# Kernel tuning notes

Hardware: AMD Instinct MI355X
Metric: run time of the kernel (lower is better)

## Reference

```python
import jax, jax.numpy as jnp
import numpy as np
from jax import lax

K = 3  # deform kernel size (forced by shape consistency of the offset branch)


def conv2d(x, w, b, pad):
    y = lax.conv_general_dilated(x, w, (1, 1), [(pad, pad), (pad, pad)],
                                 dimension_numbers=('NCHW', 'OIHW', 'NCHW'))
    return y + b[None, :, None, None]


def deform_conv(x, offset, w):
    # Deformable conv v1, stride 1, pad 0, per-group offsets, zero outside borders.
    B, Cin, H, W = x.shape
    Cout = w.shape[0]
    Ho, Wo = H - K + 1, W - K + 1
    G = offset.shape[1] // (2 * K * K)  # num deformable groups (= cin // c_p_g)
    cpg = Cin // G
    # offset layout: [B, G, K*K, 2(y,x), Ho, Wo]
    off = offset.reshape(B, G, K * K, 2, Ho, Wo)
    ky = (jnp.arange(K * K) // K).astype(x.dtype)
    kx = (jnp.arange(K * K) % K).astype(x.dtype)
    py = off[:, :, :, 0] + jnp.arange(Ho, dtype=x.dtype)[None, None, None, :, None] + ky[None, None, :, None, None]
    px = off[:, :, :, 1] + jnp.arange(Wo, dtype=x.dtype)[None, None, None, None, :] + kx[None, None, :, None, None]
    y0 = jnp.floor(py)
    x0 = jnp.floor(px)
    fy = (py - y0)[..., None]  # [B,G,KK,Ho,Wo,1]
    fx = (px - x0)[..., None]
    y0i = y0.astype(jnp.int32)
    x0i = x0.astype(jnp.int32)
    xr = x.reshape(B, G, cpg, H, W)
    bi = jnp.arange(B)[:, None, None, None, None]
    gi = jnp.arange(G)[None, :, None, None, None]

    def gather(iy, ix):
        valid = (iy >= 0) & (iy < H) & (ix >= 0) & (ix < W)
        v = xr[bi, gi, :, jnp.clip(iy, 0, H - 1), jnp.clip(ix, 0, W - 1)]  # [B,G,KK,Ho,Wo,cpg]
        return v * valid[..., None].astype(x.dtype)

    v = ((1 - fy) * (1 - fx) * gather(y0i, x0i)
         + (1 - fy) * fx * gather(y0i, x0i + 1)
         + fy * (1 - fx) * gather(y0i + 1, x0i)
         + fy * fx * gather(y0i + 1, x0i + 1))
    # [B,G,KK,Ho,Wo,cpg] -> [B, Cin*K*K, Ho, Wo] matching weight layout [Cout, Cin, K, K]
    cols = v.transpose(0, 1, 5, 2, 3, 4).reshape(B, Cin * K * K, Ho, Wo)
    return jnp.einsum('ok,bkhw->bohw', w.reshape(Cout, -1), cols)


def setup_inputs() -> dict:
    key = jax.random.key(0)
    ks = jax.random.split(key, 8)
    B, cin, cout, H, W = 4, 64, 64, 130, 130
    s = 0.05
    x = jax.random.normal(ks[0], (B, cin, H, W), jnp.float32)
    w0 = jax.random.normal(ks[1], (cin, cin, 3, 3), jnp.float32) * s
    b0 = jnp.zeros((cin,), jnp.float32)
    w1 = jax.random.normal(ks[2], (cin // 2, cin, 1, 1), jnp.float32) * s
    b1 = jnp.zeros((cin // 2,), jnp.float32)
    w2 = jax.random.normal(ks[3], (cin // 2, cin // 2, 3, 3), jnp.float32) * s
    b2 = jnp.zeros((cin // 2,), jnp.float32)
    off_ch = cin * 2 * K * K  # c_p_g = 1 -> G = cin
    w3 = jax.random.normal(ks[4], (off_ch, cin // 2, 1, 1), jnp.float32) * s
    b3 = jnp.zeros((off_ch,), jnp.float32)
    wd = jax.random.normal(ks[5], (cout, cin, K, K), jnp.float32) * s
    return {"x": x, "w0": w0, "b0": b0, "w1": w1, "b1": b1, "w2": w2, "b2": b2,
            "w3": w3, "b3": b3, "wd": wd}


def reference(x, w0, b0, w1, b1, w2, b2, w3, b3, wd):
    t = conv2d(x, w0, b0, 0)                                   # [B,cin,H-2,W-2]
    t = lax.reduce_window(t, -jnp.inf, lax.max, (1, 1, 2, 2), (1, 1, 2, 2), 'VALID')
    t = conv2d(t, w1, b1, 0)
    t = conv2d(t, w2, b2, 1)
    t = conv2d(t, w3, b3, 0)                                   # offset logits
    t = jnp.repeat(jnp.repeat(t, 2, axis=2), 2, axis=3)        # nearest x2 upsample
    return deform_conv(x, t, wd)
```

## Files before the change

kernel.cpp:

```cpp
#include <hip/hip_runtime.h>
#include <hip/hip_bf16.h>
#include <hip/hip_fp16.h>


#define HX 130
#define WX 130

typedef short bf16x8 __attribute__((ext_vector_type(8)));
typedef _Float16 f16x8 __attribute__((ext_vector_type(8)));
typedef float f32x4 __attribute__((ext_vector_type(4)));

static __device__ __forceinline__ unsigned short f2bf(float f) {
    unsigned u = __float_as_uint(f);
    unsigned r = u + 0x7fff + ((u >> 16) & 1);
    return (unsigned short)(r >> 16);
}

static __device__ __forceinline__ int aoff320(int row, int col) {
    return row * 320 + ((((col >> 3) ^ (row & 7))) << 3) + (col & 7);
}

static __device__ __forceinline__ int aoff192(int row, int col) {
    return row * 192 + ((((col >> 3) ^ (row & 7))) << 3) + (col & 7);
}

static __device__ __forceinline__ int aoff80(int row, int col) {
    return row * 80 + ((((col >> 3) ^ (row & 7))) << 3) + (col & 7);
}

__global__ __launch_bounds__(256) void k_wdt(const float* __restrict__ wd,
                                             const float* __restrict__ w3,
                                             const float* __restrict__ w0,
                                             const float* __restrict__ w2,
                                             const float* __restrict__ w1,
                                             unsigned short* __restrict__ wdtb,
                                             __half* __restrict__ w3h,
                                             unsigned short* __restrict__ w0b,
                                             unsigned short* __restrict__ w2b,
                                             unsigned short* __restrict__ w1b) {
    int idx = blockIdx.x * 256 + threadIdx.x;
    if (idx < 36864) {
        int o = idx / 576;
        int rem = idx - o * 576;
        int c = rem / 9;
        int kk = rem - c * 9;
        int h = c >> 5;
        int c5 = c & 31;
        int col = (c5 >> 4) * 144 + ((c5 >> 3) & 1) * 72 + (c5 & 7) * 9 + kk;
        wdtb[(size_t)(h * 64 + o) * 288 + col] = f2bf(wd[idx]);
        if (idx < 16) wdtb[36864 + idx] = 0;
    } else if (idx < 73728) {
        int i2 = idx - 36864;
        w3h[i2] = __float2half_rn(w3[i2]);
    } else if (idx < 114688) {
        int i3 = idx - 73728;
        int row = i3 / 160;
        int col = i3 - row * 160;
        int cig = row >> 6, oc = row & 63;
        unsigned short v = 0;
        if (col < 144) {
            int ci = (col * 57) >> 9;
            int kk = col - ci * 9;
            v = f2bf(w0[(size_t)(oc * 64 + cig * 16 + ci) * 9 + kk]);
        }
        w0b[i3] = v;
    } else if (idx < 124928) {
        int i4 = idx - 114688;
        int row = i4 / 160;
        int col = i4 - row * 160;
        int cig = row >> 5, oc = row & 31;
        unsigned short v = 0;
        if (col < 144) {
            int ci = (col * 57) >> 9;
            int kk = col - ci * 9;
            v = f2bf(w2[(size_t)(oc * 32 + cig * 16 + ci) * 9 + kk]);
        }
        w2b[i4] = v;
    } else {
        int i5 = idx - 124928;
        w1b[i5] = f2bf(w1[i5]);
    }
}

__global__ __launch_bounds__(256, 4) void k_conv0_mfma(const float* __restrict__ x,
                                                       const unsigned short* __restrict__ w0b,
                                                       const float* __restrict__ b0,
                                                       float* __restrict__ p1) {
    int blk = blockIdx.x;
    int tx = blk & 15;
    int ty = (blk >> 4) & 15;
    int b = blk >> 8;
    int tid = threadIdx.x;
    int w = tid >> 6;
    int lane = tid & 63;
    int lm = lane & 15;
    int lq = lane >> 4;
    int oy0 = ty * 8, ox0 = tx * 8;

    __shared__ __align__(16) unsigned short alds[64 * 192];
    __shared__ __align__(16) float xlds[1600];

    f32x4 acc[4];
    #pragma unroll
    for (int n = 0; n < 4; ++n) acc[n] = (f32x4){0.f, 0.f, 0.f, 0.f};

    if (tid < 128) {
        *(bf16x8*)&alds[aoff192(tid >> 1, 144 + (tid & 1) * 8)] =
            (bf16x8){0, 0, 0, 0, 0, 0, 0, 0};
    }

    const float* xb = x + (size_t)(b * 64) * (HX * WX) + oy0 * WX + ox0;
    int apx = tid >> 2;
    int acq = tid & 3;
    int py = apx >> 3, pxx = apx & 7;

    for (int cig = 0; cig < 4; ++cig) {
        #pragma unroll
        for (int j = 0; j < 7; ++j) {
            int i = tid + j * 256;
            if (i < 1600) {
                int ci = i / 100;
                int rem = i - ci * 100;
                int rr = rem / 10, cc = rem - rr * 10;
                xlds[i] = xb[(size_t)(cig * 16 + ci) * (HX * WX) + rr * WX + cc];
            }
        }
        __syncthreads();
        #pragma unroll
        for (int jj = 0; jj < 36; ++jj) {
            int col = acq * 36 + jj;
            int ci = (col * 57) >> 9;
            int kk = col - ci * 9;
            int ky = kk / 3, kx = kk - ky * 3;
            alds[aoff192(apx, col)] =
                f2bf(xlds[ci * 100 + (py + ky) * 10 + (pxx + kx)]);
        }
        __syncthreads();
        int arow = w * 16 + lm;
        const unsigned short* bbase = w0b + (size_t)cig * 64 * 160;
        #pragma unroll
        for (int ks = 0; ks < 5; ++ks) {
            bf16x8 a = *(const bf16x8*)&alds[aoff192(arow, ks * 32 + lq * 8)];
            #pragma unroll
            for (int n = 0; n < 4; ++n) {
                bf16x8 bb = *(const bf16x8*)(bbase + (size_t)(n * 16 + lm) * 160
                                             + ks * 32 + lq * 8);
                acc[n] = __builtin_amdgcn_mfma_f32_16x16x32_bf16(a, bb, acc[n], 0, 0, 0);
            }
        }
    }

    __syncthreads();
    float* dlds = (float*)alds;
    #pragma unroll
    for (int n = 0; n < 4; ++n) {
        int oc = n * 16 + lm;
        #pragma unroll
        for (int r = 0; r < 4; ++r) {
            int px = w * 16 + lq * 4 + r;
            dlds[oc * 65 + px] = acc[n][r];
        }
    }
    __syncthreads();
    {
        int oc = tid >> 2;
        int ppy = tid & 3;
        float bo = b0[oc];
        float4 o4;
        #pragma unroll
        for (int ppx = 0; ppx < 4; ++ppx) {
            const float* dp = &dlds[oc * 65 + (2 * ppy) * 8 + 2 * ppx];
            float m = fmaxf(fmaxf(dp[0], dp[1]), fmaxf(dp[8], dp[9])) + bo;
            ((float*)&o4)[ppx] = m;
        }
        *(float4*)(p1 + (((size_t)b * 64 + oc) * 64 + ty * 4 + ppy) * 64 + tx * 4) = o4;
    }
}

__global__ __launch_bounds__(256) void k_conv13(const float* __restrict__ p1,
                                                const unsigned short* __restrict__ w1b,
                                                const float* __restrict__ b1,
                                                const unsigned short* __restrict__ w2b,
                                                const float* __restrict__ b2,
                                                float* __restrict__ t3) {
    int blk = blockIdx.x;
    int tx = blk & 7;
    int ty = (blk >> 3) & 7;
    int b = blk >> 6;
    int tid = threadIdx.x;
    int w = tid >> 6;
    int lane = tid & 63;
    int lm = lane & 15;
    int lq = lane >> 4;
    int oy0 = ty * 8, ox0 = tx * 8;

    __shared__ __align__(16) float t2b[32 * 100];
    __shared__ __align__(16) unsigned short areg[64 * 192];

    const float* pb = p1 + (size_t)(b * 64) * 4096;
    #pragma unroll
    for (int j = 0; j < 25; ++j) {
        int i = tid + j * 256;
        int ci = i / 100;
        int pp = i - ci * 100;
        int rr = pp / 10, cc = pp - rr * 10;
        int gy = oy0 + rr - 1, gx = ox0 + cc - 1;
        bool ok = (gy >= 0) & (gy < 64) & (gx >= 0) & (gx < 64);
        float v = ok ? pb[(size_t)ci * 4096 + gy * 64 + gx] : 0.f;
        areg[aoff80(pp, ci)] = f2bf(v);
    }
    __syncthreads();

    #pragma unroll
    for (int s7 = 0; s7 < 2; ++s7) {
        int rt = w + s7 * 4;
        if (rt < 7) {
            f32x4 a1[2];
            a1[0] = (f32x4){0.f, 0.f, 0.f, 0.f};
            a1[1] = (f32x4){0.f, 0.f, 0.f, 0.f};
            #pragma unroll
            for (int ks = 0; ks < 2; ++ks) {
                bf16x8 a = *(const bf16x8*)&areg[aoff80(rt * 16 + lm, ks * 32 + lq * 8)];
                #pragma unroll
                for (int n = 0; n < 2; ++n) {
                    bf16x8 bb = *(const bf16x8*)(w1b + (size_t)(n * 16 + lm) * 64
                                                 + ks * 32 + lq * 8);
                    a1[n] = __builtin_amdgcn_mfma_f32_16x16x32_bf16(a, bb, a1[n], 0, 0, 0);
                }
            }
            #pragma unroll
            for (int n = 0; n < 2; ++n) {
                int oc = n * 16 + lm;
                float bv = b1[oc];
                #pragma unroll
                for (int r = 0; r < 4; ++r) {
                    int px = rt * 16 + lq * 4 + r;
                    if (px < 100) t2b[oc * 100 + px] = a1[n][r] + bv;
                }
            }
        }
    }
    __syncthreads();

    int apx = tid >> 2, acq = tid & 3;
    int py = apx >> 3, pxx = apx & 7;
    f32x4 acc3[2];
    acc3[0] = (f32x4){0.f, 0.f, 0.f, 0.f};
    acc3[1] = (f32x4){0.f, 0.f, 0.f, 0.f};
    if (tid < 128) {
        *(bf16x8*)&areg[aoff192(tid >> 1, 144 + (tid & 1) * 8)] =
            (bf16x8){0, 0, 0, 0, 0, 0, 0, 0};
    }
    #pragma unroll 1
    for (int cig = 0; cig < 2; ++cig) {
        __syncthreads();
        #pragma unroll
        for (int jj = 0; jj < 36; ++jj) {
            int col = acq * 36 + jj;
            int ci = (col * 57) >> 9;
            int kk = col - ci * 9;
            int ky = kk / 3, kx = kk - ky * 3;
            areg[aoff192(apx, col)] =
                f2bf(t2b[(cig * 16 + ci) * 100 + (py + ky) * 10 + (pxx + kx)]);
        }
        __syncthreads();
        int arow = w * 16 + lm;
        const unsigned short* bbase = w2b + (size_t)cig * 32 * 160;
        #pragma unroll
        for (int ks = 0; ks < 5; ++ks) {
            bf16x8 a = *(const bf16x8*)&areg[aoff192(arow, ks * 32 + lq * 8)];
            #pragma unroll
            for (int n = 0; n < 2; ++n) {
                bf16x8 bb = *(const bf16x8*)(bbase + (size_t)(n * 16 + lm) * 160
                                             + ks * 32 + lq * 8);
                acc3[n] = __builtin_amdgcn_mfma_f32_16x16x32_bf16(a, bb, acc3[n], 0, 0, 0);
            }
        }
    }

    __syncthreads();
    float* dlds = (float*)areg;
    #pragma unroll
    for (int n = 0; n < 2; ++n) {
        int oc = n * 16 + lm;
        #pragma unroll
        for (int r = 0; r < 4; ++r) {
            int px = w * 16 + lq * 4 + r;
            dlds[oc * 65 + px] = acc3[n][r];
        }
    }
    __syncthreads();
    {
        int oc = tid >> 3;
        int r = tid & 7;
        float bo = b2[oc];
        const float* dp = &dlds[oc * 65 + r * 8];
        float* op = t3 + ((size_t)(b * 32 + oc) * 64 + oy0 + r) * 64 + ox0;
        float4 a4 = make_float4(dp[0] + bo, dp[1] + bo, dp[2] + bo, dp[3] + bo);
        float4 b4 = make_float4(dp[4] + bo, dp[5] + bo, dp[6] + bo, dp[7] + bo);
        *(float4*)(op) = a4;
        *(float4*)(op + 4) = b4;
    }
}

__global__ __launch_bounds__(256, 3) void k_deform(const float* __restrict__ x,
                                                   const float* __restrict__ t3,
                                                   const __half* __restrict__ w3h,
                                                   const float* __restrict__ b3,
                                                   const unsigned short* __restrict__ wdtb,
                                                   float* __restrict__ out) {
    int blk = blockIdx.x;
    int k8 = blk & 7;
    int j8 = blk >> 3;
    int b = k8 & 3;
    int strip = j8 * 2 + (k8 >> 2);
    int tid = threadIdx.x;
    int po0 = strip * 16;
    int qy = po0 >> 6;
    int qx0 = po0 & 63;
    int w = tid >> 6;
    int lane = tid & 63;
    int lm = lane & 15;
    int lq = lane >> 4;
    int tq = tid & 15;
    int kb = tid >> 4;

    __shared__ __align__(16) unsigned short alds[64 * 320];
    __shared__ __align__(16) __half2 soff[2304];
    __shared__ __align__(16) _Float16 st3t[16 * 40];

    f32x4 acc[4];
    #pragma unroll
    for (int n = 0; n < 4; ++n) acc[n] = (f32x4){0.f, 0.f, 0.f, 0.f};

    const float* xb = x + (size_t)b * 64 * HX * WX;
    float fybase = (float)(2 * qy);
    float fxbase = (float)(2 * (qx0 + tq));

    {
        int px = tid & 15, ci0 = tid >> 4;
        const float* t3p = t3 + (size_t)b * 32 * 4096 + (qy * 64 + qx0 + px);
        st3t[px * 40 + ci0]      = (_Float16)t3p[(size_t)ci0 * 4096];
        st3t[px * 40 + ci0 + 16] = (_Float16)t3p[(size_t)(ci0 + 16) * 4096];
    }
    __syncthreads();
    const f16x8 bfrag = *(const f16x8*)&st3t[lm * 40 + lq * 8];

    for (int h = 0; h < 2; ++h) {
        #pragma unroll 1
        for (int sl = 0; sl < 2; ++sl) {
            int s = h * 2 + sl;
            __syncthreads();

            #pragma unroll
            for (int rep = 0; rep < 5; ++rep) {
                int t = rep * 4 + w;
                if (rep == 4) { if (w >= 2) break; t = 16 + w; }
                const f16x8 afrag = *(const f16x8*)((const _Float16*)w3h
                        + (size_t)(s * 288 + t * 16 + lm) * 32 + lq * 8);
                f32x4 d = __builtin_amdgcn_mfma_f32_16x16x32_f16(
                        afrag, bfrag, (f32x4){0.f, 0.f, 0.f, 0.f}, 0, 0, 0);
                float4 bq = *(const float4*)(b3 + s * 288 + t * 16 + lq * 4);
                int p0 = (t * 8 + lq * 2) * 16 + lm;
                soff[p0]      = __floats2half2_rn(d[0] + bq.x, d[1] + bq.y);
                soff[p0 + 16] = __floats2half2_rn(d[2] + bq.z, d[3] + bq.w);
            }
            __syncthreads();

            __half2 o2h[9];
            #pragma unroll
            for (int it = 0; it < 9; ++it)
                o2h[it] = soff[it * 256 + tid];
            #pragma unroll
            for (int it = 0; it < 9; ++it) {
                int kcol = it * 16 + kb;
                int lc = kcol >= 72;
                int ckk = kcol - 72 * lc;
                int ch = (ckk * 57) >> 9;
                int kk = ckk - ch * 9;
                int c = s * 16 + lc * 8 + ch;
                int clocal = sl * 144 + kcol;
                float2 off = __half22float2(o2h[it]);
                float py = off.x + fybase + (float)(kk / 3);
                float px = off.y + fxbase + (float)(kk % 3);
                float y0f = floorf(py), x0f = floorf(px);
                float fy = py - y0f, fx = px - x0f;
                int y0 = (int)y0f, x0 = (int)x0f;
                const float* xp = xb + (size_t)c * (HX * WX);
                float tv[3][3];
                bool fastok = (y0 >= 0) & (y0 <= HX - 3) & (x0 >= 0) & (x0 <= WX - 3);
                if (__all(fastok)) {
                    int xe = x0 & ~1;
                    int odd = x0 & 1;
                    const float* rp = xp + y0 * WX + xe;
                    #pragma unroll
                    for (int r = 0; r < 3; ++r) {
                        float2 A = *(const float2*)(rp);
                        float2 B = *(const float2*)(rp + 2);
                        tv[r][0] = odd ? A.y : A.x;
                        tv[r][1] = odd ? B.x : A.y;
                        tv[r][2] = odd ? B.y : B.x;
                        rp += WX;
                    }
                } else {
                    #pragma unroll
                    for (int r = 0; r < 3; ++r) {
                        int yy = y0 + r;
                        bool vy = (yy >= 0) & (yy < HX);
                        int yc = min(max(yy, 0), HX - 1);
                        #pragma unroll
                        for (int sx = 0; sx < 3; ++sx) {
                            int xx = x0 + sx;
                            bool vx = (xx >= 0) & (xx < WX);
                            int xc = min(max(xx, 0), WX - 1);
                            float val = xp[yc * WX + xc];
                            tv[r][sx] = (vy & vx) ? val : 0.f;
                        }
                    }
                }
                float h0[3], h1[3];
                #pragma unroll
                for (int r = 0; r < 3; ++r) {
                    h0[r] = tv[r][0] + fx * (tv[r][1] - tv[r][0]);
                    h1[r] = tv[r][1] + fx * (tv[r][2] - tv[r][1]);
                }
                alds[aoff320(0 * 16 + tq, clocal)] = f2bf(h0[0] + fy * (h0[1] - h0[0]));
                alds[aoff320(1 * 16 + tq, clocal)] = f2bf(h1[0] + fy * (h1[1] - h1[0]));
                alds[aoff320(2 * 16 + tq, clocal)] = f2bf(h0[1] + fy * (h0[2] - h0[1]));
                alds[aoff320(3 * 16 + tq, clocal)] = f2bf(h1[1] + fy * (h1[2] - h1[1]));
            }
        }
        __syncthreads();

        int arow = w * 16 + lm;
        const unsigned short* bbase = wdtb + (size_t)(h * 64) * 288;
        __builtin_amdgcn_s_setprio(1);
        #pragma unroll
        for (int ks = 0; ks < 9; ++ks) {
            bf16x8 a = *(const bf16x8*)&alds[aoff320(arow, ks * 32 + lq * 8)];
            #pragma unroll
            for (int n = 0; n < 4; ++n) {
                bf16x8 bb = *(const bf16x8*)(bbase + (size_t)(n * 16 + lm) * 288
                                             + ks * 32 + lq * 8);
                acc[n] = __builtin_amdgcn_mfma_f32_16x16x32_bf16(a, bb, acc[n], 0, 0, 0);
            }
        }
        __builtin_amdgcn_s_setprio(0);
    }

    __syncthreads();
    float* dlds = (float*)alds;
    #pragma unroll
    for (int n = 0; n < 4; ++n) {
        int oc = n * 16 + lm;
        #pragma unroll
        for (int r = 0; r < 4; ++r) {
            int px = w * 16 + lq * 4 + r;
            dlds[oc * 65 + px] = acc[n][r];
        }
    }
    __syncthreads();
    {
        int oc = tid >> 2;
        int sy = (tid >> 1) & 1;
        int qh = (tid & 1) * 8;
        float* orow = out + (((size_t)b * 64 + oc) * 128 + 2 * qy + sy) * 128 + 2 * qx0;
        const float* d0 = &dlds[oc * 65 + (sy * 2 + 0) * 16];
        const float* d1 = &dlds[oc * 65 + (sy * 2 + 1) * 16];
        #pragma unroll
        for (int i = 0; i < 8; ++i) {
            int q = qh + i;
            *(float2*)(orow + 2 * q) = make_float2(d0[q], d1[q]);
        }
    }
}

extern "C" void kernel_launch(void* const* d_in, const int* in_sizes, int n_in,
                              void* d_out, int out_size, void* d_ws, size_t ws_size,
                              hipStream_t stream) {
    const float* x  = (const float*)d_in[0];
    const float* w0 = (const float*)d_in[1];
    const float* b0 = (const float*)d_in[2];
    const float* w1 = (const float*)d_in[3];
    const float* b1 = (const float*)d_in[4];
    const float* w2 = (const float*)d_in[5];
    const float* b2 = (const float*)d_in[6];
    const float* w3 = (const float*)d_in[7];
    const float* b3 = (const float*)d_in[8];
    const float* wd = (const float*)d_in[9];
    float* out = (float*)d_out;

    float* ws = (float*)d_ws;
    float* p1    = ws;
    float* t3    = p1 + 1048576;
    unsigned short* wdtb = (unsigned short*)(t3 + 524288);
    __half* w3h = (__half*)(wdtb + 36880);
    unsigned short* w0b = (unsigned short*)(w3h + 36864);
    unsigned short* w2b = w0b + 40960;
    unsigned short* w1b = w2b + 10240;

    k_wdt<<<496, 256, 0, stream>>>(wd, w3, w0, w2, w1, wdtb, w3h, w0b, w2b, w1b);
    k_conv0_mfma<<<1024, 256, 0, stream>>>(x, w0b, b0, p1);
    k_conv13<<<256, 256, 0, stream>>>(p1, w1b, b1, w2b, b2, t3);
    k_deform<<<1024, 256, 0, stream>>>(x, t3, w3h, b3, wdtb, out);
}
```

Baseline: 223.2 us.

## Compute offsets per wave via MFMA and lane shuffles, dropping the offset LDS staging

Each wave now computes the offset-logit MFMA tiles it needs directly and redistributes them with cross-lane shuffles, replacing the shared-memory soff staging buffer and its two block barriers per slice. Offsets stay in fp32 rather than being rounded to half, and the bias is added per thread. In exchange, each wave issues more redundant MFMAs (9 per slice instead of about 4-5) and 36 shuffles. A barrier is also moved inside the h loop so the LDS tile is protected before the next slice's writes.

```diff
diff --git a/kernel.cpp b/kernel.cpp
--- a/kernel.cpp
+++ b/kernel.cpp
@@ -310,10 +310,10 @@
                                                    const unsigned short* __restrict__ wdtb,
                                                    float* __restrict__ out) {
     int blk = blockIdx.x;
-    int k8 = blk & 7;
+    int k8x = blk & 7;
     int j8 = blk >> 3;
-    int b = k8 & 3;
-    int strip = j8 * 2 + (k8 >> 2);
+    int b = k8x & 3;
+    int strip = j8 * 2 + (k8x >> 2);
     int tid = threadIdx.x;
     int po0 = strip * 16;
     int qy = po0 >> 6;
@@ -326,7 +326,6 @@
     int kb = tid >> 4;
 
     __shared__ __align__(16) unsigned short alds[64 * 320];
-    __shared__ __align__(16) __half2 soff[2304];
     __shared__ __align__(16) _Float16 st3t[16 * 40];
 
     f32x4 acc[4];
@@ -336,6 +335,11 @@
     const float* xb = x + (size_t)b * 64 * HX * WX;
     float fybase = (float)(2 * qy);
     float fxbase = (float)(2 * (qx0 + tq));
+
+    int k8 = kb & 7;
+    int srcl = ((k8 >> 1) << 4) | tq;
+    int odd_k = k8 & 1;
+    int tpar = kb >> 3;
 
     {
         int px = tid & 15, ci0 = tid >> 4;
@@ -350,39 +354,29 @@
         #pragma unroll 1
         for (int sl = 0; sl < 2; ++sl) {
             int s = h * 2 + sl;
-            __syncthreads();
-
             #pragma unroll
-            for (int rep = 0; rep < 5; ++rep) {
-                int t = rep * 4 + w;
-                if (rep == 4) { if (w >= 2) break; t = 16 + w; }
+            for (int it = 0; it < 9; ++it) {
+                int t = 2 * it + tpar;
                 const f16x8 afrag = *(const f16x8*)((const _Float16*)w3h
                         + (size_t)(s * 288 + t * 16 + lm) * 32 + lq * 8);
                 f32x4 d = __builtin_amdgcn_mfma_f32_16x16x32_f16(
                         afrag, bfrag, (f32x4){0.f, 0.f, 0.f, 0.f}, 0, 0, 0);
-                float4 bq = *(const float4*)(b3 + s * 288 + t * 16 + lq * 4);
-                int p0 = (t * 8 + lq * 2) * 16 + lm;
-                soff[p0]      = __floats2half2_rn(d[0] + bq.x, d[1] + bq.y);
-                soff[p0 + 16] = __floats2half2_rn(d[2] + bq.z, d[3] + bq.w);
-            }
-            __syncthreads();
-
-            __half2 o2h[9];
-            #pragma unroll
-            for (int it = 0; it < 9; ++it)
-                o2h[it] = soff[it * 256 + tid];
-            #pragma unroll
-            for (int it = 0; it < 9; ++it) {
+                float v0 = __shfl(d[0], srcl, 64);
+                float v1 = __shfl(d[1], srcl, 64);
+                float v2 = __shfl(d[2], srcl, 64);
+                float v3 = __shfl(d[3], srcl, 64);
+                float pyr = odd_k ? v2 : v0;
+                float pxr = odd_k ? v3 : v1;
                 int kcol = it * 16 + kb;
+                float2 bq2 = *(const float2*)(b3 + s * 288 + 2 * kcol);
                 int lc = kcol >= 72;
                 int ckk = kcol - 72 * lc;
                 int ch = (ckk * 57) >> 9;
                 int kk = ckk - ch * 9;
                 int c = s * 16 + lc * 8 + ch;
                 int clocal = sl * 144 + kcol;
-                float2 off = __half22float2(o2h[it]);
-                float py = off.x + fybase + (float)(kk / 3);
-                float px = off.y + fxbase + (float)(kk % 3);
+                float py = pyr + bq2.x + fybase + (float)(kk / 3);
+                float px = pxr + bq2.y + fxbase + (float)(kk % 3);
                 float y0f = floorf(py), x0f = floorf(px);
                 float fy = py - y0f, fx = px - x0f;
                 int y0 = (int)y0f, x0 = (int)x0f;
@@ -446,9 +440,9 @@
             }
         }
         __builtin_amdgcn_s_setprio(0);
-    }
-
-    __syncthreads();
+        __syncthreads();
+    }
+
     float* dlds = (float*)alds;
     #pragma unroll
     for (int n = 0; n < 4; ++n) {
```

After: 229.5 us. 2.8% more time.
